# Optimization experiments

Measured on AMD Instinct MI355X. Metric: run time of the kernel, lower is better.

The kernel has to match this reference:

```python
import jax, jax.numpy as jnp
import numpy as np

B, I, H = 4096, 512, 1024


def setup_inputs() -> dict:
    key = jax.random.key(0)
    ks = jax.random.split(key, 22)
    inp = {
        "y": jax.random.normal(ks[0], (B, I), jnp.float32),
        "h_light": jax.random.normal(ks[1], (B, H), jnp.float32),
        "c_light": jax.random.normal(ks[2], (B, H), jnp.float32),
        "h_temp": jax.random.normal(ks[3], (B, H), jnp.float32),
        "c_temp": jax.random.normal(ks[4], (B, H), jnp.float32),
    }
    names = ["w_f_light", "w_i_light", "w_c_light", "w_o_light",
             "w_f_light_temp", "w_i_light_temp", "w_c_light_temp", "w_o_light_temp"]
    for j, n in enumerate(names):
        inp[n] = jax.random.normal(ks[5 + j], (H, H + I), jnp.float32) * 0.02
        inp["b" + n[1:]] = jax.random.normal(ks[13 + j], (H,), jnp.float32) * 0.02
    return inp


def _branch(hx, wf, bf, wi, bi, wc, bc, wo, bo):
    # Fuse the 4 gate GEMMs of one branch into a single [B, H+I] x [H+I, 4H] matmul
    W = jnp.concatenate([wf, wi, wc, wo], axis=0)            # [4H, H+I]
    b = jnp.concatenate([bf, bi, bc, bo], axis=0)            # [4H]
    z = hx @ W.T + b                                         # [B, 4H]
    zf, zi, zc, zo = jnp.split(z, 4, axis=1)
    return jax.nn.sigmoid(zf), jax.nn.sigmoid(zi), jnp.tanh(zc), jax.nn.sigmoid(zo)


def reference(y, h_light, c_light, h_temp, c_temp,
              w_f_light, b_f_light, w_i_light, b_i_light,
              w_c_light, b_c_light, w_o_light, b_o_light,
              w_f_light_temp, b_f_light_temp, w_i_light_temp, b_i_light_temp,
              w_c_light_temp, b_c_light_temp, w_o_light_temp, b_o_light_temp):
    hx_l = jnp.concatenate([h_light, y], axis=1)  # [B, H+I]
    hx_t = jnp.concatenate([h_temp, y], axis=1)   # [B, H+I]
    f1, i1, ch1, o1 = _branch(hx_l, w_f_light, b_f_light, w_i_light, b_i_light,
                              w_c_light, b_c_light, w_o_light, b_o_light)
    f2, i2, ch2, o2 = _branch(hx_t, w_f_light_temp, b_f_light_temp, w_i_light_temp,
                              b_i_light_temp, w_c_light_temp, b_c_light_temp,
                              w_o_light_temp, b_o_light_temp)
    c_new = (f1 * c_light + i1 * ch1) + (f2 * c_light + i2 * ch2)
    h_new = (o1 + o2) * jnp.tanh(c_new)
    return h_new, c_new
```

## Files before the change

kernel.cpp:

```cpp
#include <hip/hip_runtime.h>
#include <stdint.h>


#define B_DIM 4096
#define I_DIM 512
#define H_DIM 1024
#define K_DIM 1536
#define NK 48
#define BUFB (48 * 1024)

typedef __attribute__((ext_vector_type(8))) __bf16 bf16x8;
typedef __attribute__((ext_vector_type(4))) float f32x4;
typedef __attribute__((ext_vector_type(4))) uint32_t u32x4;

static __device__ __forceinline__ uint32_t f2bf(float f) {
  uint32_t u = __builtin_bit_cast(uint32_t, f);
  return (u + 0x7FFFu + ((u >> 16) & 1u)) >> 16;
}
static __device__ __forceinline__ uint32_t pack2(float lo, float hi) {
  return f2bf(lo) | (f2bf(hi) << 16);
}
static __device__ __forceinline__ float sigf(float x) {
  return 1.f / (1.f + __expf(-x));
}
static __device__ __forceinline__ float tanhfast(float x) {
  float t = __expf(fminf(2.f * x, 80.f));
  return (t - 1.f) / (t + 1.f);
}

__global__ __launch_bounds__(192) void convert_kernel(
    const float* __restrict__ y, const float* __restrict__ h_light,
    const float* __restrict__ h_temp,
    const float* __restrict__ w0, const float* __restrict__ w1,
    const float* __restrict__ w2, const float* __restrict__ w3,
    const float* __restrict__ w4, const float* __restrict__ w5,
    const float* __restrict__ w6, const float* __restrict__ w7,
    uint16_t* __restrict__ ws)
{
  const int row_all = blockIdx.x;
  const int cs = threadIdx.x;
  const int cl = (cs & ~3) | ((cs & 3) ^ ((row_all >> 1) & 3));
  const int k0 = cl * 8;
  const float* src;
  if (row_all < 2 * B_DIM) {
    const int branch = row_all >> 12;
    const int row = row_all & (B_DIM - 1);
    const float* hb = branch ? h_temp : h_light;
    src = (k0 < H_DIM) ? (hb + (size_t)row * H_DIM + k0)
                       : (y + (size_t)row * I_DIM + (k0 - H_DIM));
  } else {
    const int ra = row_all - 2 * B_DIM;
    const int mat = ra >> 10;
    const int row = ra & (H_DIM - 1);
    const float* w = (mat < 4) ? ((mat < 2) ? (mat == 0 ? w0 : w1) : (mat == 2 ? w2 : w3))
                               : ((mat < 6) ? (mat == 4 ? w4 : w5) : (mat == 6 ? w6 : w7));
    src = w + (size_t)row * K_DIM + k0;
  }
  f32x4 v0 = *(const f32x4*)src;
  f32x4 v1 = *(const f32x4*)(src + 4);
  u32x4 o;
  o[0] = pack2(v0[0], v0[1]);
  o[1] = pack2(v0[2], v0[3]);
  o[2] = pack2(v1[0], v1[1]);
  o[3] = pack2(v1[2], v1[3]);
  *(u32x4*)(ws + ((size_t)row_all * 192 + cs) * 8) = o;
}

__global__ __launch_bounds__(512, 2) void lstm_fused_kernel(
    const uint16_t* __restrict__ ws,
    const float* __restrict__ c_light,
    const float* __restrict__ bf1, const float* __restrict__ bi1,
    const float* __restrict__ bc1, const float* __restrict__ bo1,
    const float* __restrict__ bf2, const float* __restrict__ bi2,
    const float* __restrict__ bc2, const float* __restrict__ bo2,
    float* __restrict__ out)
{
  __shared__ alignas(128) char smem[3 * BUFB];

  const int tid = threadIdx.x;
  const int lane = tid & 63;
  const int wv = tid >> 6;

  const int bid = blockIdx.x;
  const int wg = (bid & 7) * 64 + (bid >> 3);
  const int bm0 = (wg >> 4) * 128;
  const int bn0 = (wg & 15) * 64;

  const uint16_t* wsA = ws;
  const uint16_t* wsW = ws + (size_t)2 * B_DIM * K_DIM;

  const int rA = lane & 15;
  const int kg = lane >> 4;
  const uint32_t fo = (uint32_t)rA * 64u + (uint32_t)((kg ^ ((rA >> 1) & 3))) * 16u;

  const uint16_t* sA0;
  const uint16_t* sA1;
  const uint16_t* sB[4];
  {
    int c = tid;
    sA0 = wsA + (size_t)(bm0 + ((c >> 2) & 127)) * K_DIM + (c & 3) * 8;
    c = 512 + tid;
    sA1 = wsA + (size_t)B_DIM * K_DIM + (size_t)(bm0 + ((c >> 2) & 127)) * K_DIM + (c & 3) * 8;
#pragma unroll
    for (int j = 0; j < 4; ++j) {
      int c2 = j * 512 + tid;
      sB[j] = wsW + (size_t)(c2 >> 8) * ((size_t)H_DIM * K_DIM) +
              (size_t)(bn0 + ((c2 >> 2) & 63)) * K_DIM + (c2 & 3) * 8;
    }
  }
  const uint32_t ldA0 = (uint32_t)tid * 16u;
  const uint32_t ldA1 = (uint32_t)(512 + tid) * 16u;
  uint32_t ldB[4];
#pragma unroll
  for (int j = 0; j < 4; ++j) ldB[j] = (uint32_t)(1024 + j * 512 + tid) * 16u;

  const uint32_t aBase = (uint32_t)(wv >> 2) * 8192u;
  const uint32_t bBase = 16384u + (uint32_t)wv * 4096u;

#define ISSUE(srcp, ldsoff, tg)                                              \
  __builtin_amdgcn_global_load_lds(                                          \
      (const __attribute__((address_space(1))) void*)(srcp),                 \
      (__attribute__((address_space(3))) void*)(&smem[(size_t)(tg)*BUFB + (ldsoff)]), \
      16, 0, 0)

  f32x4 acc[8][4];
#pragma unroll
  for (int m = 0; m < 8; ++m)
#pragma unroll
    for (int n = 0; n < 4; ++n) acc[m][n] = (f32x4){0.f, 0.f, 0.f, 0.f};

  ISSUE(sA0, ldA0, 0); ISSUE(sA1, ldA1, 0);
#pragma unroll
  for (int j = 0; j < 4; ++j) ISSUE(sB[j], ldB[j], 0);
  ISSUE(sA0 + 32, ldA0, 1); ISSUE(sA1 + 32, ldA1, 1);
#pragma unroll
  for (int j = 0; j < 4; ++j) ISSUE(sB[j] + 32, ldB[j], 1);
  sA0 += 64; sA1 += 64;
#pragma unroll
  for (int j = 0; j < 4; ++j) sB[j] += 64;
  asm volatile("s_waitcnt vmcnt(6)" ::: "memory");
  __builtin_amdgcn_s_barrier();

  for (int kt = 0; kt < NK; ++kt) {
    const int bi = kt % 3;
    const int tg = (bi == 0) ? 2 : bi - 1;
    const char* As = smem + (size_t)bi * BUFB + aBase;
    const char* Bs = smem + (size_t)bi * BUFB + bBase;
    const bool pf = (kt + 2 < NK);

    bf16x8 Af[4], Bf[4];
#pragma unroll
    for (int m = 0; m < 4; ++m) Af[m] = *(const bf16x8*)(As + m * 1024 + fo);
#pragma unroll
    for (int n = 0; n < 4; ++n) Bf[n] = *(const bf16x8*)(Bs + n * 1024 + fo);
    if (pf) { ISSUE(sA0, ldA0, tg); ISSUE(sA1, ldA1, tg); ISSUE(sB[0], ldB[0], tg); }
    __builtin_amdgcn_s_barrier();
    asm volatile("s_waitcnt lgkmcnt(0)" ::: "memory");
    __builtin_amdgcn_s_setprio(1);
#pragma unroll
    for (int m = 0; m < 4; ++m)
#pragma unroll
      for (int n = 0; n < 4; ++n)
        acc[m][n] = __builtin_amdgcn_mfma_f32_16x16x32_bf16(Af[m], Bf[n], acc[m][n], 0, 0, 0);
    __builtin_amdgcn_s_setprio(0);
    __builtin_amdgcn_s_barrier();

    bf16x8 Ag[4];
#pragma unroll
    for (int m = 0; m < 4; ++m) Ag[m] = *(const bf16x8*)(As + (m + 4) * 1024 + fo);
    if (pf) { ISSUE(sB[1], ldB[1], tg); ISSUE(sB[2], ldB[2], tg); ISSUE(sB[3], ldB[3], tg); }
    __builtin_amdgcn_s_barrier();
    asm volatile("s_waitcnt lgkmcnt(0)" ::: "memory");
    __builtin_amdgcn_s_setprio(1);
#pragma unroll
    for (int m = 0; m < 4; ++m)
#pragma unroll
      for (int n = 0; n < 4; ++n)
        acc[m + 4][n] = __builtin_amdgcn_mfma_f32_16x16x32_bf16(Ag[m], Bf[n], acc[m + 4][n], 0, 0, 0);
    __builtin_amdgcn_s_setprio(0);
    if (kt + 2 < NK) asm volatile("s_waitcnt vmcnt(6)" ::: "memory");
    else             asm volatile("s_waitcnt vmcnt(0)" ::: "memory");
    __builtin_amdgcn_s_barrier();

    sA0 += 32; sA1 += 32;
#pragma unroll
    for (int j = 0; j < 4; ++j) sB[j] += 32;
  }
#undef ISSUE

  float* zst = (float*)smem;
#pragma unroll
  for (int q = 0; q < 4; ++q) {
    __syncthreads();
#pragma unroll
    for (int mm = 0; mm < 2; ++mm)
#pragma unroll
      for (int n = 0; n < 4; ++n)
#pragma unroll
        for (int j = 0; j < 4; ++j) {
          int r = mm * 16 + kg * 4 + j;
          int c = n * 16 + rA;
          zst[wv * 2176 + r * 68 + c] = acc[q * 2 + mm][n][j];
        }
    __syncthreads();

    int r = tid >> 4;
    int cb = (tid & 15) * 4;
    int grow = bm0 + q * 32 + r;
    int gc = bn0 + cb;
    const float* zb = zst + r * 68 + cb;
    f32x4 z0 = *(const f32x4*)(zb + 0 * 2176) + *(const f32x4*)(bf1 + gc);
    f32x4 z1 = *(const f32x4*)(zb + 1 * 2176) + *(const f32x4*)(bi1 + gc);
    f32x4 z2 = *(const f32x4*)(zb + 2 * 2176) + *(const f32x4*)(bc1 + gc);
    f32x4 z3 = *(const f32x4*)(zb + 3 * 2176) + *(const f32x4*)(bo1 + gc);
    f32x4 z4 = *(const f32x4*)(zb + 4 * 2176) + *(const f32x4*)(bf2 + gc);
    f32x4 z5 = *(const f32x4*)(zb + 5 * 2176) + *(const f32x4*)(bi2 + gc);
    f32x4 z6 = *(const f32x4*)(zb + 6 * 2176) + *(const f32x4*)(bc2 + gc);
    f32x4 z7 = *(const f32x4*)(zb + 7 * 2176) + *(const f32x4*)(bo2 + gc);
    f32x4 cl4 = *(const f32x4*)(c_light + (size_t)grow * H_DIM + gc);
    f32x4 hv, cv;
#pragma unroll
    for (int j = 0; j < 4; ++j) {
      float f1 = sigf(z0[j]);
      float i1 = sigf(z1[j]);
      float ch1 = tanhfast(z2[j]);
      float o1 = sigf(z3[j]);
      float f2 = sigf(z4[j]);
      float i2 = sigf(z5[j]);
      float ch2 = tanhfast(z6[j]);
      float o2 = sigf(z7[j]);
      float cn = f1 * cl4[j] + i1 * ch1 + f2 * cl4[j] + i2 * ch2;
      hv[j] = (o1 + o2) * tanhfast(cn);
      cv[j] = cn;
    }
    *(f32x4*)(out + (size_t)grow * H_DIM + gc) = hv;
    *(f32x4*)(out + (size_t)(B_DIM * H_DIM) + (size_t)grow * H_DIM + gc) = cv;
  }
}

extern "C" void kernel_launch(void* const* d_in, const int* in_sizes, int n_in,
                              void* d_out, int out_size, void* d_ws, size_t ws_size,
                              hipStream_t stream) {
  (void)in_sizes; (void)n_in; (void)out_size; (void)ws_size;
  const float* y       = (const float*)d_in[0];
  const float* h_light = (const float*)d_in[1];
  const float* c_light = (const float*)d_in[2];
  const float* h_temp  = (const float*)d_in[3];
  uint16_t* ws = (uint16_t*)d_ws;

  convert_kernel<<<16384, 192, 0, stream>>>(
      y, h_light, h_temp,
      (const float*)d_in[5],  (const float*)d_in[7],  (const float*)d_in[9],  (const float*)d_in[11],
      (const float*)d_in[13], (const float*)d_in[15], (const float*)d_in[17], (const float*)d_in[19],
      ws);

  lstm_fused_kernel<<<512, 512, 0, stream>>>(
      ws, c_light,
      (const float*)d_in[6],  (const float*)d_in[8],  (const float*)d_in[10], (const float*)d_in[12],
      (const float*)d_in[14], (const float*)d_in[16], (const float*)d_in[18], (const float*)d_in[20],
      (float*)d_out);
}
```

Before: 303.1 us.

## Restructure GEMM main loop to one barrier per K-step with grouped prefetch

Collapses the two half-steps of each K iteration into one. All 8 A fragments and 4 B fragments are now read from LDS up front, all six async global→LDS prefetches are issued together, and a single vmcnt wait plus barrier sits at the top of the loop instead of four barriers. Prefetch addresses are computed from the iteration index instead of incrementing pointers. This cuts synchronisation overhead but gives up the interleaving of LDS reads with MFMA work, and raises register pressure.

```diff
diff --git a/kernel.cpp b/kernel.cpp
--- a/kernel.cpp
+++ b/kernel.cpp
@@ -135,56 +135,37 @@
   ISSUE(sA0 + 32, ldA0, 1); ISSUE(sA1 + 32, ldA1, 1);
 #pragma unroll
   for (int j = 0; j < 4; ++j) ISSUE(sB[j] + 32, ldB[j], 1);
-  sA0 += 64; sA1 += 64;
-#pragma unroll
-  for (int j = 0; j < 4; ++j) sB[j] += 64;
-  asm volatile("s_waitcnt vmcnt(6)" ::: "memory");
-  __builtin_amdgcn_s_barrier();
 
   for (int kt = 0; kt < NK; ++kt) {
+    if (kt < NK - 1) asm volatile("s_waitcnt vmcnt(6)" ::: "memory");
+    else             asm volatile("s_waitcnt vmcnt(0)" ::: "memory");
+    __builtin_amdgcn_s_barrier();
+
     const int bi = kt % 3;
-    const int tg = (bi == 0) ? 2 : bi - 1;
     const char* As = smem + (size_t)bi * BUFB + aBase;
     const char* Bs = smem + (size_t)bi * BUFB + bBase;
-    const bool pf = (kt + 2 < NK);
-
-    bf16x8 Af[4], Bf[4];
-#pragma unroll
-    for (int m = 0; m < 4; ++m) Af[m] = *(const bf16x8*)(As + m * 1024 + fo);
+
+    bf16x8 Af[8], Bf[4];
+#pragma unroll
+    for (int m = 0; m < 8; ++m) Af[m] = *(const bf16x8*)(As + m * 1024 + fo);
 #pragma unroll
     for (int n = 0; n < 4; ++n) Bf[n] = *(const bf16x8*)(Bs + n * 1024 + fo);
-    if (pf) { ISSUE(sA0, ldA0, tg); ISSUE(sA1, ldA1, tg); ISSUE(sB[0], ldB[0], tg); }
-    __builtin_amdgcn_s_barrier();
-    asm volatile("s_waitcnt lgkmcnt(0)" ::: "memory");
+
+    if (kt + 2 < NK) {
+      const int tg = (bi == 0) ? 2 : bi - 1;
+      const uint32_t ko = (uint32_t)(kt + 2) * 32u;
+      ISSUE(sA0 + ko, ldA0, tg);   ISSUE(sA1 + ko, ldA1, tg);
+      ISSUE(sB[0] + ko, ldB[0], tg); ISSUE(sB[1] + ko, ldB[1], tg);
+      ISSUE(sB[2] + ko, ldB[2], tg); ISSUE(sB[3] + ko, ldB[3], tg);
+    }
+
     __builtin_amdgcn_s_setprio(1);
 #pragma unroll
-    for (int m = 0; m < 4; ++m)
+    for (int m = 0; m < 8; ++m)
 #pragma unroll
       for (int n = 0; n < 4; ++n)
         acc[m][n] = __builtin_amdgcn_mfma_f32_16x16x32_bf16(Af[m], Bf[n], acc[m][n], 0, 0, 0);
     __builtin_amdgcn_s_setprio(0);
-    __builtin_amdgcn_s_barrier();
-
-    bf16x8 Ag[4];
-#pragma unroll
-    for (int m = 0; m < 4; ++m) Ag[m] = *(const bf16x8*)(As + (m + 4) * 1024 + fo);
-    if (pf) { ISSUE(sB[1], ldB[1], tg); ISSUE(sB[2], ldB[2], tg); ISSUE(sB[3], ldB[3], tg); }
-    __builtin_amdgcn_s_barrier();
-    asm volatile("s_waitcnt lgkmcnt(0)" ::: "memory");
-    __builtin_amdgcn_s_setprio(1);
-#pragma unroll
-    for (int m = 0; m < 4; ++m)
-#pragma unroll
-      for (int n = 0; n < 4; ++n)
-        acc[m + 4][n] = __builtin_amdgcn_mfma_f32_16x16x32_bf16(Ag[m], Bf[n], acc[m + 4][n], 0, 0, 0);
-    __builtin_amdgcn_s_setprio(0);
-    if (kt + 2 < NK) asm volatile("s_waitcnt vmcnt(6)" ::: "memory");
-    else             asm volatile("s_waitcnt vmcnt(0)" ::: "memory");
-    __builtin_amdgcn_s_barrier();
-
-    sA0 += 32; sA1 += 32;
-#pragma unroll
-    for (int j = 0; j < 4; ++j) sB[j] += 32;
   }
 #undef ISSUE
 
```

Result: no change. 303.6 us (+0.2%).
